# Performance work log

Measured on AMD Instinct MI355X. Metric: run time of the kernel, lower is better.

Reference implementation:

```python
import jax, jax.numpy as jnp
import numpy as np

NUM_CLASSES = 2
THRESHOLD = 0.5
NEGPOS_RATIO = 3
VAR0, VAR1 = 0.1, 0.2  # self.variance = [0.1, 0.2]


def point_form(priors):
    # [cx,cy,w,h] -> [xmin,ymin,xmax,ymax]
    return jnp.concatenate([priors[:, :2] - priors[:, 2:] / 2,
                            priors[:, :2] + priors[:, 2:] / 2], axis=1)


def jaccard(a, b):
    # a: [O,4], b: [P,4] point-form -> IoU [O,P]
    tl = jnp.maximum(a[:, None, :2], b[None, :, :2])
    br = jnp.minimum(a[:, None, 2:], b[None, :, 2:])
    wh = jnp.clip(br - tl, 0.0)
    inter = wh[..., 0] * wh[..., 1]
    area_a = ((a[:, 2] - a[:, 0]) * (a[:, 3] - a[:, 1]))[:, None]
    area_b = ((b[:, 2] - b[:, 0]) * (b[:, 3] - b[:, 1]))[None, :]
    return inter / (area_a + area_b - inter)


def encode(matched, priors):
    # matched: [P,4] point-form GT, priors: [P,4] center-size
    g_cxcy = ((matched[:, :2] + matched[:, 2:]) / 2 - priors[:, :2]) / (VAR0 * priors[:, 2:])
    g_wh = jnp.log((matched[:, 2:] - matched[:, :2]) / priors[:, 2:]) / VAR1
    return jnp.concatenate([g_cxcy, g_wh], axis=1)


def match_one(truths, labels, priors):
    # truths: [O,4], labels: [O], priors: [P,4]
    O = truths.shape[0]
    overlaps = jaccard(truths, point_form(priors))          # [O,P]
    best_prior_idx = jnp.argmax(overlaps, axis=1)           # [O] best prior per GT
    best_truth_overlap = jnp.max(overlaps, axis=0)          # [P]
    best_truth_idx = jnp.argmax(overlaps, axis=0)           # [P]
    # ensure each GT keeps its best prior
    best_truth_overlap = best_truth_overlap.at[best_prior_idx].set(2.0)
    best_truth_idx = best_truth_idx.at[best_prior_idx].set(jnp.arange(O))
    matches = truths[best_truth_idx]                        # [P,4]
    conf = labels[best_truth_idx].astype(jnp.int32)         # head label == 1
    conf = jnp.where(best_truth_overlap < THRESHOLD, 0, conf)
    loc = encode(matches, priors)                           # [P,4]
    return loc, conf


def setup_inputs() -> dict:
    key = jax.random.key(0)
    k1, k2, k3, k4, k5, k6 = jax.random.split(key, 6)
    B, P, O = 32, 32768, 32
    loc_data = jax.random.normal(k1, (B, P, 3), jnp.float32) * 0.1
    conf_data = jax.random.normal(k2, (B, P, 2), jnp.float32)
    cxy = jax.random.uniform(k3, (P, 2), jnp.float32, 0.1, 0.9)
    wh = jax.random.uniform(k4, (P, 2), jnp.float32, 0.05, 0.2)
    priors = jnp.concatenate([cxy, wh], axis=1)
    xy1 = jax.random.uniform(k5, (B, O, 2), jnp.float32, 0.0, 0.7)
    twh = jax.random.uniform(k6, (B, O, 2), jnp.float32, 0.05, 0.25)
    targets = jnp.concatenate([xy1, xy1 + twh, jnp.ones((B, O, 1), jnp.float32)], axis=2)
    return {"loc_data": loc_data, "conf_data": conf_data, "priors": priors, "targets": targets}


def reference(loc_data, conf_data, priors, targets):
    B, P, _ = loc_data.shape
    # convert_coord: [cx, cy, gw] -> [cx, cy, gw, gw]
    quard = jnp.stack([loc_data[..., 0], loc_data[..., 1],
                       loc_data[..., 2], loc_data[..., 2]], axis=-1)  # [B,P,4]
    truths = targets[..., :4]
    labels = targets[..., 4]
    loc_t, conf_t = jax.vmap(lambda t, l: match_one(t, l, priors))(truths, labels)
    pos = conf_t > 0                                         # [B,P]
    # localization smooth-L1 over positives (sum reduction)
    d = quard - loc_t
    ad = jnp.abs(d)
    sl1 = jnp.where(ad < 1.0, 0.5 * d * d, ad - 0.5)
    loss_l = jnp.sum(sl1 * pos[..., None].astype(sl1.dtype))
    # per-prior CE for hard-negative mining
    lse = jax.nn.logsumexp(conf_data, axis=-1)               # [B,P]
    picked = jnp.take_along_axis(conf_data, conf_t[..., None], axis=-1)[..., 0]
    ce = lse - picked                                        # [B,P]
    ce_mine = jnp.where(pos, 0.0, ce)
    # double argsort -> rank of each prior by mining loss (descending)
    loss_idx = jnp.argsort(-ce_mine, axis=1)
    idx_rank = jnp.argsort(loss_idx, axis=1)
    num_pos = jnp.sum(pos.astype(jnp.int32), axis=1, keepdims=True)  # [B,1]
    num_neg = jnp.minimum(NEGPOS_RATIO * num_pos, P - 1)
    neg = idx_rank < num_neg
    sel = jnp.logical_or(pos, neg)
    loss_c = jnp.sum(jnp.where(sel, ce, 0.0))
    N = jnp.sum(num_pos).astype(loss_l.dtype)
    return loss_l / N, loss_c / N
```

## Files before the change

kernel.cpp:

```cpp
#include <hip/hip_runtime.h>
#include <math.h>

#define Bn 32
#define Pn 32768
#define On 32
#define TPB 256
#define PPT 4
#define BP  (TPB * PPT)
#define AG 8
#define AC 1024


__device__ __forceinline__ unsigned long long shfl_down_u64(unsigned long long v, int off) {
    unsigned lo = (unsigned)(v & 0xFFFFFFFFull);
    unsigned hi = (unsigned)(v >> 32);
    lo = __shfl_down(lo, off, 64);
    hi = __shfl_down(hi, off, 64);
    return ((unsigned long long)hi << 32) | lo;
}

__global__ __launch_bounds__(256) void matchA(const float4* __restrict__ priors,
                                              const float* __restrict__ targets,
                                              unsigned long long* __restrict__ bpm) {
    int g    = blockIdx.x;
    int base = blockIdx.y * AC;
    int tid  = threadIdx.x;

    __shared__ float4 tb[AG];
    __shared__ float  ta[AG];
    __shared__ unsigned long long sbest[AG];

    if (tid < AG) {
        const float* t = targets + (size_t)(g * AG + tid) * 5;
        float x1 = t[0], y1 = t[1], x2 = t[2], y2 = t[3];
        tb[tid] = make_float4(x1, y1, x2, y2);
        ta[tid] = (x2 - x1) * (y2 - y1);
        sbest[tid] = 0ull;
    }
    __syncthreads();

    float px1[4], py1[4], px2[4], py2[4], ab[4];
#pragma unroll
    for (int j = 0; j < 4; j++) {
        float4 pr = priors[base + tid + 256 * j];
        px1[j] = pr.x - pr.z * 0.5f; py1[j] = pr.y - pr.w * 0.5f;
        px2[j] = pr.x + pr.z * 0.5f; py2[j] = pr.y + pr.w * 0.5f;
        ab[j]  = (px2[j] - px1[j]) * (py2[j] - py1[j]);
    }

#pragma unroll
    for (int o = 0; o < AG; o++) {
        float4 tt = tb[o];
        float  a  = ta[o];
        float bI = 0.f, bU = 1.f;
        int   bj = 0;
#pragma unroll
        for (int j = 0; j < 4; j++) {
            float ix1 = fmaxf(tt.x, px1[j]), iy1 = fmaxf(tt.y, py1[j]);
            float ix2 = fminf(tt.z, px2[j]), iy2 = fminf(tt.w, py2[j]);
            float iw = fmaxf(ix2 - ix1, 0.f), ih = fmaxf(iy2 - iy1, 0.f);
            float I = iw * ih;
            float U = a + ab[j] - I;
            if (I * bU > bI * U) { bI = I; bU = U; bj = j; }
        }
        int p = base + tid + 256 * bj;
        float iou = bI / bU;
        unsigned long long key = ((unsigned long long)__float_as_uint(iou) << 32)
                               | (unsigned)(Pn - 1 - p);
#pragma unroll
        for (int off = 32; off > 0; off >>= 1) {
            unsigned long long other = shfl_down_u64(key, off);
            if (other > key) key = other;
        }
        if ((tid & 63) == 0) atomicMax(&sbest[o], key);
    }
    __syncthreads();
    if (tid < AG) atomicMax(&bpm[g * AG + tid], sbest[tid]);
}

__global__ __launch_bounds__(256) void matchB(const float* __restrict__ loc,
                                              const float2* __restrict__ conf2,
                                              const float4* __restrict__ priors,
                                              const float* __restrict__ targets,
                                              const unsigned long long* __restrict__ bpm,
                                              float* __restrict__ ce_mine,
                                              int* __restrict__ num_pos,
                                              float* __restrict__ loss_l_t,
                                              float* __restrict__ ce_t,
                                              int* __restrict__ np_tot) {
    int b = blockIdx.y;
    int base = blockIdx.x * BP;
    int tid = threadIdx.x;

    float2 cc[PPT];
#pragma unroll
    for (int j = 0; j < PPT; j++) cc[j] = conf2[(size_t)b * Pn + base + tid + 256 * j];

    __shared__ float4 tb[On];
    __shared__ float  ta[On], lb[On];
    __shared__ int    forced[BP];
    __shared__ float  sred[12];

#pragma unroll
    for (int j = 0; j < PPT; j++) forced[tid + 256 * j] = -1;
    int sp = -1;
    if (tid < On) {
        const float* t = targets + ((size_t)b * On + tid) * 5;
        float x1 = t[0], y1 = t[1], x2 = t[2], y2 = t[3];
        tb[tid] = make_float4(x1, y1, x2, y2);
        ta[tid] = (x2 - x1) * (y2 - y1);
        lb[tid] = t[4];
        sp = Pn - 1 - (int)(bpm[b * On + tid] & 0xFFFFFFFFull);
    }
    __syncthreads();
    if (tid < On && sp >= base && sp < base + BP)
        atomicMax(&forced[sp - base], tid);
    __syncthreads();

    float px1[PPT], py1[PPT], px2[PPT], py2[PPT], ab[PPT], pcx[PPT], pcy[PPT], pw[PPT], ph[PPT];
#pragma unroll
    for (int j = 0; j < PPT; j++) {
        float4 pr = priors[base + tid + 256 * j];
        pcx[j] = pr.x; pcy[j] = pr.y; pw[j] = pr.z; ph[j] = pr.w;
        px1[j] = pr.x - pr.z * 0.5f; py1[j] = pr.y - pr.w * 0.5f;
        px2[j] = pr.x + pr.z * 0.5f; py2[j] = pr.y + pr.w * 0.5f;
        ab[j]  = (px2[j] - px1[j]) * (py2[j] - py1[j]);
    }

    float bIc[PPT][2], bUc[PPT][2];
    int   bxc[PPT][2];
#pragma unroll
    for (int j = 0; j < PPT; j++)
#pragma unroll
        for (int h = 0; h < 2; h++) { bIc[j][h] = 0.f; bUc[j][h] = 1.f; bxc[j][h] = h * 16; }

#pragma unroll 2
    for (int o16 = 0; o16 < 16; o16++) {
#pragma unroll
        for (int h = 0; h < 2; h++) {
            int o = h * 16 + o16;
            float4 tt = tb[o];
            float  a  = ta[o];
#pragma unroll
            for (int j = 0; j < PPT; j++) {
                float ix1 = fmaxf(tt.x, px1[j]), iy1 = fmaxf(tt.y, py1[j]);
                float ix2 = fminf(tt.z, px2[j]), iy2 = fminf(tt.w, py2[j]);
                float iw = fmaxf(ix2 - ix1, 0.f), ih = fmaxf(iy2 - iy1, 0.f);
                float I = iw * ih;
                float U = a + ab[j] - I;
                if (I * bUc[j][h] > bIc[j][h] * U) { bIc[j][h] = I; bUc[j][h] = U; bxc[j][h] = o; }
            }
        }
    }
    float bI[PPT], bU[PPT];
    int   bx[PPT];
#pragma unroll
    for (int j = 0; j < PPT; j++) {
        bI[j] = bIc[j][0]; bU[j] = bUc[j][0]; bx[j] = bxc[j][0];
        if (bIc[j][1] * bU[j] > bI[j] * bUc[j][1]) { bI[j] = bIc[j][1]; bU[j] = bUc[j][1]; bx[j] = bxc[j][1]; }
    }

    float ll_s = 0.f, pce_s = 0.f, cnt_s = 0.f;
#pragma unroll
    for (int j = 0; j < PPT; j++) {
        int p = base + tid + 256 * j;
        int fo = forced[tid + 256 * j];
        int bidx = (fo >= 0) ? fo : bx[j];
        int cf;
        if (fo >= 0)                      cf = (int)lb[bidx];
        else if (bI[j] >= 0.5f * bU[j])   cf = (int)lb[bidx];
        else                              cf = 0;
        bool pos = cf > 0;

        if (pos) {
            float4 tt = tb[bidx];
            float g0 = ((tt.x + tt.z) * 0.5f - pcx[j]) / (0.1f * pw[j]);
            float g1 = ((tt.y + tt.w) * 0.5f - pcy[j]) / (0.1f * ph[j]);
            float g2 = __logf((tt.z - tt.x) / pw[j]) * 5.0f;
            float g3 = __logf((tt.w - tt.y) / ph[j]) * 5.0f;
            const float* lp = loc + ((size_t)b * Pn + p) * 3;
            float q0 = lp[0], q1 = lp[1], q2 = lp[2];
            float dd[4] = { q0 - g0, q1 - g1, q2 - g2, q2 - g3 };
#pragma unroll
            for (int i = 0; i < 4; i++) {
                float ad = fabsf(dd[i]);
                ll_s += (ad < 1.f) ? 0.5f * dd[i] * dd[i] : (ad - 0.5f);
            }
            cnt_s += 1.f;
        }

        float m = fmaxf(cc[j].x, cc[j].y);
        float lse = m + __logf(__expf(cc[j].x - m) + __expf(cc[j].y - m));
        float ce = lse - (cf ? cc[j].y : cc[j].x);
        if (pos) { pce_s += ce; ce = 0.f; }
        ce_mine[(size_t)b * Pn + p] = fmaxf(ce, 0.f);
    }

#pragma unroll
    for (int off = 32; off > 0; off >>= 1) {
        ll_s  += __shfl_down(ll_s,  off, 64);
        pce_s += __shfl_down(pce_s, off, 64);
        cnt_s += __shfl_down(cnt_s, off, 64);
    }
    int lane = tid & 63, wv = tid >> 6;
    if (lane == 0) { sred[wv * 3] = ll_s; sred[wv * 3 + 1] = pce_s; sred[wv * 3 + 2] = cnt_s; }
    __syncthreads();
    if (tid == 0) {
        float llr = 0, pcer = 0, cntr = 0;
        for (int w = 0; w < 4; w++) { llr += sred[w*3]; pcer += sred[w*3+1]; cntr += sred[w*3+2]; }
        if (llr != 0.f)  atomicAdd(loss_l_t, llr);
        if (pcer != 0.f) atomicAdd(ce_t, pcer);
        int c = (int)cntr;
        if (c) { atomicAdd(&num_pos[b], c); atomicAdd(np_tot, c); }
    }
}

__global__ __launch_bounds__(1024) void topk(const float* __restrict__ ce_mine,
                                             const int* __restrict__ num_pos,
                                             float* __restrict__ ce_t,
                                             const float* __restrict__ loss_l_t,
                                             const int* __restrict__ np_tot,
                                             unsigned* __restrict__ tick,
                                             float* __restrict__ out) {
    int b = blockIdx.x, tid = threadIdx.x;
    const float4* v4 = (const float4*)(ce_mine + (size_t)b * Pn);
    float4 r[8];
#pragma unroll
    for (int i = 0; i < 8; i++) r[i] = v4[i * 1024 + tid];

    int k = 3 * num_pos[b];
    if (k > Pn - 1) k = Pn - 1;

    __shared__ int hist[8192];
    __shared__ int wavetot[16];
    __shared__ int waveabove[16];
    __shared__ unsigned long long wcand[16];
    __shared__ unsigned s_lo;
    __shared__ int s_ab;
    __shared__ float ssum[16];
    __shared__ int   scnt[16];

    int lane = tid & 63, wv = tid >> 6;

    if (k > 0) {
        unsigned LO = 0u;
        int AB = 0;

        const int SH[3] = {22, 11, 0};
        const int NB[3] = {512, 2048, 2048};

#pragma unroll
        for (int rd = 0; rd < 3; rd++) {
            int shift = SH[rd], nb = NB[rd];
            int nsub = (rd == 0) ? 16 : 4;
#pragma unroll
            for (int i = 0; i < 8; i++) hist[tid + 1024 * i] = 0;
            __syncthreads();
            int* myh = (rd == 0) ? (hist + (wv << 9)) : (hist + ((wv >> 2) << 11));
#pragma unroll
            for (int i = 0; i < 8; i++) {
                float4 rv = r[i];
                float vals[4] = {rv.x, rv.y, rv.z, rv.w};
#pragma unroll
                for (int q = 0; q < 4; q++) {
                    unsigned u = __float_as_uint(vals[q]);
                    unsigned bin = (u - LO) >> shift;
                    if (bin < (unsigned)nb) atomicAdd(&myh[bin], 1);
                }
            }
            __syncthreads();
            bool own = (2 * tid) < nb;
            int c0 = 0, c1 = 0;
            if (own) {
                for (int s = 0; s < nsub; s++) {
                    c0 += hist[s * nb + 2 * tid];
                    c1 += hist[s * nb + 2 * tid + 1];
                }
            }
            int suf = c0 + c1;
#pragma unroll
            for (int off = 1; off < 64; off <<= 1) {
                int src = lane + off;
                int o = __shfl(suf, src & 63, 64);
                suf += (src < 64) ? o : 0;
            }
            if (lane == 0) wavetot[wv] = suf;
            __syncthreads();
            if (wv == 0) {
                int t = (lane < 16) ? wavetot[lane] : 0;
#pragma unroll
                for (int off = 1; off < 16; off <<= 1) {
                    int o2 = __shfl(t, (lane + off) & 63, 64);
                    t += ((lane + off) < 16) ? o2 : 0;
                }
                if (lane < 16) waveabove[lane] = AB + t - wavetot[lane];
            }
            __syncthreads();
            int S0 = waveabove[wv] + suf;
            int S1 = S0 - c0;
            int cand = -1; unsigned nab = 0;
            if (own && S0 >= k) { cand = 2*tid;     nab = (unsigned)(S0 - c0); }
            if (own && S1 >= k) { cand = 2*tid + 1; nab = (unsigned)(S1 - c1); }
            unsigned long long pk = ((unsigned long long)(unsigned)(cand + 1) << 32) | nab;
#pragma unroll
            for (int off = 32; off > 0; off >>= 1) {
                unsigned long long o = shfl_down_u64(pk, off);
                if (o > pk) pk = o;
            }
            if (lane == 0) wcand[wv] = pk;
            __syncthreads();
            if (wv == 0) {
                unsigned long long pk2 = (lane < 16) ? wcand[lane] : 0ull;
#pragma unroll
                for (int off = 1; off < 16; off <<= 1) {
                    unsigned long long o2 = shfl_down_u64(pk2, off);
                    if (o2 > pk2) pk2 = o2;
                }
                if (lane == 0) {
                    int ci = (int)(pk2 >> 32) - 1;
                    s_lo = LO + ((unsigned)ci << shift);
                    s_ab = (int)(pk2 & 0xFFFFFFFFu);
                }
            }
            __syncthreads();
            LO = s_lo; AB = s_ab;
        }
        float tau = __uint_as_float(LO);
        float s = 0.f; int c = 0;
#pragma unroll
        for (int i = 0; i < 8; i++) {
            if (r[i].x > tau) { s += r[i].x; c++; }
            if (r[i].y > tau) { s += r[i].y; c++; }
            if (r[i].z > tau) { s += r[i].z; c++; }
            if (r[i].w > tau) { s += r[i].w; c++; }
        }
#pragma unroll
        for (int off = 32; off > 0; off >>= 1) {
            s += __shfl_down(s, off, 64);
            c += __shfl_down(c, off, 64);
        }
        if (lane == 0) { ssum[wv] = s; scnt[wv] = c; }
        __syncthreads();
        if (tid == 0) {
            float st = 0.f; int ct = 0;
            for (int w = 0; w < 16; w++) { st += ssum[w]; ct += scnt[w]; }
            atomicAdd(ce_t, st + (float)(k - ct) * tau);
        }
    }

    if (tid == 0) {
        __threadfence();
        unsigned done = atomicAdd(tick, 1u);
        if (done == (unsigned)(Bn - 1)) {
            float N  = (float)atomicAdd((int*)np_tot, 0);
            float ll = atomicAdd((float*)loss_l_t, 0.f);
            float ce = atomicAdd(ce_t, 0.f);
            out[0] = ll / N;
            out[1] = ce / N;
        }
    }
}

extern "C" void kernel_launch(void* const* d_in, const int* in_sizes, int n_in,
                              void* d_out, int out_size, void* d_ws, size_t ws_size,
                              hipStream_t stream) {
    const float* loc     = (const float*)d_in[0];
    const float* conf    = (const float*)d_in[1];
    const float* priors  = (const float*)d_in[2];
    const float* targets = (const float*)d_in[3];
    float* out = (float*)d_out;

    char* ws = (char*)d_ws;
    unsigned long long* bpm = (unsigned long long*)ws;
    int*   num_pos  = (int*)(ws + 8192);
    float* loss_l_t = (float*)(ws + 8320);
    float* ce_t     = (float*)(ws + 8324);
    int*   np_tot   = (int*)(ws + 8328);
    unsigned* tick  = (unsigned*)(ws + 8332);
    float* ce_mine  = (float*)(ws + 16384);

    hipMemsetAsync(ws, 0, 16384, stream);

    hipLaunchKernelGGL(matchA, dim3((Bn * On) / AG, Pn / AC), dim3(256), 0, stream,
                       (const float4*)priors, targets, bpm);
    hipLaunchKernelGGL(matchB, dim3(Pn / BP, Bn), dim3(256), 0, stream,
                       loc, (const float2*)conf, (const float4*)priors, targets, bpm,
                       ce_mine, num_pos, loss_l_t, ce_t, np_tot);
    hipLaunchKernelGGL(topk, dim3(Bn), dim3(1024), 0, stream,
                       ce_mine, num_pos, ce_t, loss_l_t, np_tot, tick, out);
}
```

Before: 160.4 us.

## Restructure matchA per batch with wave-owned GTs and simplify topk bin search

matchA now launches one block per (1024-prior chunk, batch). Each wave keeps 16 priors per lane in registers and evaluates 8 of the batch's 32 ground truths, so each prior load is reused across more truths. The per-wave shuffle reductions are interleaved and the block-level shared atomics are dropped in favour of direct global atomicMax per wave. The topk radix-select replaces its multi-wave scan over all bins with a single wave that sums four sub-histograms and scans serially. That shortens synchronisation but serialises the bin walk onto one wave, and round 0 now uses 4 sub-histograms instead of 16, so atomic contention there rises.

```diff
diff --git a/kernel.cpp b/kernel.cpp
--- a/kernel.cpp
+++ b/kernel.cpp
@@ -7,8 +7,7 @@
 #define TPB 256
 #define PPT 4
 #define BP  (TPB * PPT)
-#define AG 8
-#define AC 1024
+#define APB 1024
 
 
 __device__ __forceinline__ unsigned long long shfl_down_u64(unsigned long long v, int off) {
@@ -22,60 +21,67 @@
 __global__ __launch_bounds__(256) void matchA(const float4* __restrict__ priors,
                                               const float* __restrict__ targets,
                                               unsigned long long* __restrict__ bpm) {
-    int g    = blockIdx.x;
-    int base = blockIdx.y * AC;
+    int b    = blockIdx.y;
+    int base = blockIdx.x * APB;
     int tid  = threadIdx.x;
-
-    __shared__ float4 tb[AG];
-    __shared__ float  ta[AG];
-    __shared__ unsigned long long sbest[AG];
-
-    if (tid < AG) {
-        const float* t = targets + (size_t)(g * AG + tid) * 5;
+    int lane = tid & 63, wv = tid >> 6;
+
+    __shared__ float4 tb[On];
+    __shared__ float  ta[On];
+
+    if (tid < On) {
+        const float* t = targets + ((size_t)b * On + tid) * 5;
         float x1 = t[0], y1 = t[1], x2 = t[2], y2 = t[3];
         tb[tid] = make_float4(x1, y1, x2, y2);
         ta[tid] = (x2 - x1) * (y2 - y1);
-        sbest[tid] = 0ull;
+    }
+
+    float px1[16], py1[16], px2[16], py2[16], ab[16];
+#pragma unroll
+    for (int i = 0; i < 16; i++) {
+        float4 pr = priors[base + lane + 64 * i];
+        px1[i] = pr.x - pr.z * 0.5f; py1[i] = pr.y - pr.w * 0.5f;
+        px2[i] = pr.x + pr.z * 0.5f; py2[i] = pr.y + pr.w * 0.5f;
+        ab[i]  = (px2[i] - px1[i]) * (py2[i] - py1[i]);
     }
     __syncthreads();
 
-    float px1[4], py1[4], px2[4], py2[4], ab[4];
-#pragma unroll
-    for (int j = 0; j < 4; j++) {
-        float4 pr = priors[base + tid + 256 * j];
-        px1[j] = pr.x - pr.z * 0.5f; py1[j] = pr.y - pr.w * 0.5f;
-        px2[j] = pr.x + pr.z * 0.5f; py2[j] = pr.y + pr.w * 0.5f;
-        ab[j]  = (px2[j] - px1[j]) * (py2[j] - py1[j]);
-    }
-
-#pragma unroll
-    for (int o = 0; o < AG; o++) {
+    unsigned long long key[8];
+#pragma unroll
+    for (int t = 0; t < 8; t++) {
+        int o = wv * 8 + t;
         float4 tt = tb[o];
         float  a  = ta[o];
         float bI = 0.f, bU = 1.f;
-        int   bj = 0;
-#pragma unroll
-        for (int j = 0; j < 4; j++) {
-            float ix1 = fmaxf(tt.x, px1[j]), iy1 = fmaxf(tt.y, py1[j]);
-            float ix2 = fminf(tt.z, px2[j]), iy2 = fminf(tt.w, py2[j]);
+        int   bi = 0;
+#pragma unroll
+        for (int i = 0; i < 16; i++) {
+            float ix1 = fmaxf(tt.x, px1[i]), iy1 = fmaxf(tt.y, py1[i]);
+            float ix2 = fminf(tt.z, px2[i]), iy2 = fminf(tt.w, py2[i]);
             float iw = fmaxf(ix2 - ix1, 0.f), ih = fmaxf(iy2 - iy1, 0.f);
             float I = iw * ih;
-            float U = a + ab[j] - I;
-            if (I * bU > bI * U) { bI = I; bU = U; bj = j; }
-        }
-        int p = base + tid + 256 * bj;
+            float U = a + ab[i] - I;
+            if (I * bU > bI * U) { bI = I; bU = U; bi = i; }
+        }
+        int p = base + lane + 64 * bi;
         float iou = bI / bU;
-        unsigned long long key = ((unsigned long long)__float_as_uint(iou) << 32)
-                               | (unsigned)(Pn - 1 - p);
-#pragma unroll
-        for (int off = 32; off > 0; off >>= 1) {
-            unsigned long long other = shfl_down_u64(key, off);
-            if (other > key) key = other;
-        }
-        if ((tid & 63) == 0) atomicMax(&sbest[o], key);
-    }
-    __syncthreads();
-    if (tid < AG) atomicMax(&bpm[g * AG + tid], sbest[tid]);
+        key[t] = ((unsigned long long)__float_as_uint(iou) << 32)
+               | (unsigned)(Pn - 1 - p);
+    }
+
+#pragma unroll
+    for (int off = 32; off > 0; off >>= 1) {
+        unsigned long long other[8];
+#pragma unroll
+        for (int t = 0; t < 8; t++) other[t] = shfl_down_u64(key[t], off);
+#pragma unroll
+        for (int t = 0; t < 8; t++) if (other[t] > key[t]) key[t] = other[t];
+    }
+    if (lane == 0) {
+#pragma unroll
+        for (int t = 0; t < 8; t++)
+            atomicMax(&bpm[b * On + wv * 8 + t], key[t]);
+    }
 }
 
 __global__ __launch_bounds__(256) void matchB(const float* __restrict__ loc,
@@ -232,9 +238,6 @@
     if (k > Pn - 1) k = Pn - 1;
 
     __shared__ int hist[8192];
-    __shared__ int wavetot[16];
-    __shared__ int waveabove[16];
-    __shared__ unsigned long long wcand[16];
     __shared__ unsigned s_lo;
     __shared__ int s_ab;
     __shared__ float ssum[16];
@@ -252,11 +255,10 @@
 #pragma unroll
         for (int rd = 0; rd < 3; rd++) {
             int shift = SH[rd], nb = NB[rd];
-            int nsub = (rd == 0) ? 16 : 4;
 #pragma unroll
             for (int i = 0; i < 8; i++) hist[tid + 1024 * i] = 0;
             __syncthreads();
-            int* myh = (rd == 0) ? (hist + (wv << 9)) : (hist + ((wv >> 2) << 11));
+            int* myh = hist + ((wv >> 2) << 11);
 #pragma unroll
             for (int i = 0; i < 8; i++) {
                 float4 rv = r[i];
@@ -269,57 +271,33 @@
                 }
             }
             __syncthreads();
-            bool own = (2 * tid) < nb;
-            int c0 = 0, c1 = 0;
-            if (own) {
-                for (int s = 0; s < nsub; s++) {
-                    c0 += hist[s * nb + 2 * tid];
-                    c1 += hist[s * nb + 2 * tid + 1];
+            if (wv == 0) {
+                int bpl = nb >> 6;
+                int bb = lane * bpl;
+                int lsum = 0;
+                for (int q = 0; q < bpl; q++) {
+                    int bin = bb + q;
+                    lsum += hist[bin] + hist[2048 + bin] + hist[4096 + bin] + hist[6144 + bin];
                 }
-            }
-            int suf = c0 + c1;
-#pragma unroll
-            for (int off = 1; off < 64; off <<= 1) {
-                int src = lane + off;
-                int o = __shfl(suf, src & 63, 64);
-                suf += (src < 64) ? o : 0;
-            }
-            if (lane == 0) wavetot[wv] = suf;
-            __syncthreads();
-            if (wv == 0) {
-                int t = (lane < 16) ? wavetot[lane] : 0;
-#pragma unroll
-                for (int off = 1; off < 16; off <<= 1) {
-                    int o2 = __shfl(t, (lane + off) & 63, 64);
-                    t += ((lane + off) < 16) ? o2 : 0;
+                int suf = lsum;
+#pragma unroll
+                for (int off = 1; off < 64; off <<= 1) {
+                    int o = __shfl(suf, (lane + off) & 63, 64);
+                    suf += ((lane + off) < 64) ? o : 0;
                 }
-                if (lane < 16) waveabove[lane] = AB + t - wavetot[lane];
-            }
-            __syncthreads();
-            int S0 = waveabove[wv] + suf;
-            int S1 = S0 - c0;
-            int cand = -1; unsigned nab = 0;
-            if (own && S0 >= k) { cand = 2*tid;     nab = (unsigned)(S0 - c0); }
-            if (own && S1 >= k) { cand = 2*tid + 1; nab = (unsigned)(S1 - c1); }
-            unsigned long long pk = ((unsigned long long)(unsigned)(cand + 1) << 32) | nab;
-#pragma unroll
-            for (int off = 32; off > 0; off >>= 1) {
-                unsigned long long o = shfl_down_u64(pk, off);
-                if (o > pk) pk = o;
-            }
-            if (lane == 0) wcand[wv] = pk;
-            __syncthreads();
-            if (wv == 0) {
-                unsigned long long pk2 = (lane < 16) ? wcand[lane] : 0ull;
-#pragma unroll
-                for (int off = 1; off < 16; off <<= 1) {
-                    unsigned long long o2 = shfl_down_u64(pk2, off);
-                    if (o2 > pk2) pk2 = o2;
-                }
-                if (lane == 0) {
-                    int ci = (int)(pk2 >> 32) - 1;
-                    s_lo = LO + ((unsigned)ci << shift);
-                    s_ab = (int)(pk2 & 0xFFFFFFFFu);
+                int kk = k - AB;
+                if (suf >= kk && (suf - lsum) < kk) {
+                    int acc = suf - lsum;
+                    for (int q = bpl - 1; q >= 0; q--) {
+                        int bin = bb + q;
+                        int hc = hist[bin] + hist[2048 + bin] + hist[4096 + bin] + hist[6144 + bin];
+                        acc += hc;
+                        if (acc >= kk) {
+                            s_lo = LO + ((unsigned)bin << shift);
+                            s_ab = AB + (acc - hc);
+                            break;
+                        }
+                    }
                 }
             }
             __syncthreads();
@@ -381,7 +359,7 @@
 
     hipMemsetAsync(ws, 0, 16384, stream);
 
-    hipLaunchKernelGGL(matchA, dim3((Bn * On) / AG, Pn / AC), dim3(256), 0, stream,
+    hipLaunchKernelGGL(matchA, dim3(Pn / APB, Bn), dim3(256), 0, stream,
                        (const float4*)priors, targets, bpm);
     hipLaunchKernelGGL(matchB, dim3(Pn / BP, Bn), dim3(256), 0, stream,
                        loc, (const float2*)conf, (const float4*)priors, targets, bpm,
```

Result: no change. 161.4 us (+0.6%).
